# Performance work log

Hardware: AMD Instinct MI355X
Metric: run time of the kernel (lower is better)

The kernel has to match this reference:

```python
import jax, jax.numpy as jnp
import numpy as np
import math

EPS = 1e-06
H = W = 28


def _cell_id(cell):
    Hc, Wc = H // cell, W // cell
    yy = np.arange(H)[:, None]
    xx = np.arange(W)[None, :]
    cy = np.clip(yy // cell, 0, Hc - 1)
    cx = np.clip(xx // cell, 0, Wc - 1)
    return Hc, Wc, jnp.asarray((cy * Wc + cx).astype(np.int32))


def _sobel(x):
    # x: [B,1,28,28], zero-padded 3x3 Sobel, scaled by 1/4
    p = jnp.pad(x, ((0, 0), (0, 0), (1, 1), (1, 1)))
    gx = (p[..., :-2, :-2] + 2.0 * p[..., 1:-1, :-2] + p[..., 2:, :-2]
          - p[..., :-2, 2:] - 2.0 * p[..., 1:-1, 2:] - p[..., 2:, 2:]) * 0.25
    gy = (p[..., :-2, :-2] + 2.0 * p[..., :-2, 1:-1] + p[..., :-2, 2:]
          - p[..., 2:, :-2] - 2.0 * p[..., 2:, 1:-1] - p[..., 2:, 2:]) * 0.25
    return gx, gy


def _hog_generic(gx, gy, bins, cell, eps):
    B = gx.shape[0]
    mag = jnp.sqrt(gx * gx + gy * gy + eps)
    ang = jnp.arctan2(gy, gx) * (180.0 / math.pi)
    ang = (ang + 180.0) % 180.0
    Hc, Wc, cell_id = _cell_id(cell)
    bin_w = 180.0 / bins
    b0 = jnp.clip(jnp.floor(ang / bin_w), 0, bins - 1).astype(jnp.int32)
    frac = (ang - b0.astype(ang.dtype) * bin_w) / bin_w
    b1 = (b0 + 1) % bins
    base = (jnp.arange(B, dtype=jnp.int32) * (Hc * Wc)).reshape(B, 1, 1, 1)
    dest = base + cell_id[None, None, :, :]  # [B,1,H,W]
    m = mag.reshape(-1)
    f = frac.reshape(-1)
    d = dest.reshape(-1)
    idx0 = d * bins + b0.reshape(-1)
    idx1 = d * bins + b1.reshape(-1)
    nseg = B * Hc * Wc * bins
    # single fused scatter-add for both soft-assigned bins
    hist_1d = jax.ops.segment_sum(
        jnp.concatenate([m * (1.0 - f), m * f]),
        jnp.concatenate([idx0, idx1]),
        num_segments=nseg,
    )
    hist = hist_1d.reshape(B, Hc, Wc, bins)
    blk = jnp.stack(
        [hist[:, :-1, :-1, :], hist[:, :-1, 1:, :],
         hist[:, 1:, :-1, :], hist[:, 1:, 1:, :]],
        axis=-2,
    ).reshape(B, Hc - 1, Wc - 1, 4 * bins)
    norm = jnp.sqrt(jnp.sum(blk * blk, axis=-1, keepdims=True) + 1e-06)
    blk = jnp.minimum(blk / norm, 0.2)  # L2-hys clip
    norm2 = jnp.sqrt(jnp.sum(blk * blk, axis=-1, keepdims=True) + 1e-06)
    blk = blk / norm2
    return blk.reshape(B, -1)


def setup_inputs() -> dict:
    key = jax.random.key(0)
    k1, k2 = jax.random.split(key)
    B = 16384
    x = jax.random.uniform(k1, (B, 1, 28, 28), dtype=jnp.float32)
    feat_dim = 784 + 1152 + 2304 + 4056
    feat_mean = jnp.zeros((feat_dim,), dtype=jnp.float32)
    feat_std = jnp.ones((feat_dim,), dtype=jnp.float32)
    return {"x": x, "feat_mean": feat_mean, "feat_std": feat_std}


def reference(x, feat_mean, feat_std):
    x = x.astype(jnp.float32)
    gx, gy = _sobel(x)
    h4 = _hog_generic(gx, gy, bins=8, cell=4, eps=EPS)   # [B,1152]
    h3 = _hog_generic(gx, gy, bins=9, cell=3, eps=EPS)   # [B,2304]
    h2 = _hog_generic(gx, gy, bins=6, cell=2, eps=EPS)   # [B,4056]
    flat = x.reshape(x.shape[0], -1)                      # [B,784]
    feat = jnp.concatenate([flat, h4, h3, h2], axis=1)    # [B,8296]
    return (feat - feat_mean) / feat_std
```

## Files before the change

kernel.cpp:

```cpp
#include <hip/hip_runtime.h>
#include <hip/hip_fp16.h>
#include <math.h>


constexpr int NPIX = 784;
constexpr int FEAT = 8296;
constexpr int PB4 = 10, PB3 = 10, PB2 = 8;
constexpr int O4P = 0;
constexpr int O3P = 490;
constexpr int O2P = 1300;
constexpr int HIST_TOT = 2868;
constexpr int NTASK = 269;
constexpr int NHOG = FEAT - NPIX;
constexpr int NCELL = 49 + 81 + 196;

__device__ __forceinline__ int feat_map(int i) {
    int task, h;
    if (i < 1936) {
        int k = i - 784;
        int t = k >> 5, r = k & 31;
        int q = r >> 3, j = r & 7;
        int by = t / 6, bx = t - by * 6;
        h = O4P + ((by + (q >> 1)) * 7 + bx + (q & 1)) * PB4 + j;
        task = t;
    } else if (i < 4240) {
        int k = i - 1936;
        int t = k / 36, r = k - t * 36;
        int q = r / 9,  j = r - q * 9;
        int by = t >> 3, bx = t & 7;
        h = O3P + ((by + (q >> 1)) * 9 + bx + (q & 1)) * PB3 + j;
        task = 36 + t;
    } else {
        int k = i - 4240;
        int t = k / 24, r = k - t * 24;
        int q = r / 6,  j = r - q * 6;
        int by = t / 13, bx = t - by * 13;
        h = O2P + ((by + (q >> 1)) * 14 + bx + (q & 1)) * PB2 + j;
        task = 100 + t;
    }
    return (task << 12) | h;
}

__global__ __launch_bounds__(256)
void setup_kernel(const float* __restrict__ fmean,
                  const float* __restrict__ fstd,
                  float2* __restrict__ msr, int* __restrict__ map) {
    int i = blockIdx.x * 256 + threadIdx.x;
    if (i < FEAT) {
        msr[i] = make_float2(fmean[i], 1.0f / fstd[i]);
        if (i >= NPIX) map[i - NPIX] = feat_map(i);
    }
}

__device__ __forceinline__ float orient_deg(float gy, float gx) {
    float ax = fabsf(gx), ay = fabsf(gy);
    float mn = fminf(ax, ay), mx = fmaxf(ax, ay);
    float r = __fdividef(mn, mx + 1e-37f);
    float a = r * r;
    float th = ((((0.0208351f * a - 0.0851330f) * a + 0.1801410f) * a
                 - 0.3302995f) * a + 0.9998660f) * r;
    th *= 57.29577951308232f;
    if (ay > ax) th = 90.0f - th;
    bool neg = ((__float_as_uint(gx) ^ __float_as_uint(gy)) >> 31) != 0;
    float o = neg ? 180.0f - th : th;
    return (o >= 180.0f) ? 0.0f : o;
}

__device__ __forceinline__ float ldimg(const float* img, int y, int x) {
    return (y >= 0 && y < 28 && x >= 0 && x < 28) ? img[y * 28 + x] : 0.0f;
}

template <int BINS>
__device__ __forceinline__ float2 norm_task(const float* hist, int c00,
                                            int Wc, int pb) {
    int qb[4] = {c00, c00 + pb, c00 + Wc * pb, c00 + (Wc + 1) * pb};
    float s = 1e-6f;
    #pragma unroll
    for (int q = 0; q < 4; ++q) {
        #pragma unroll
        for (int j = 0; j < BINS / 2; ++j) {
            float2 v = *reinterpret_cast<const float2*>(&hist[qb[q] + 2 * j]);
            s += v.x * v.x + v.y * v.y;
        }
        if (BINS & 1) {
            float v = hist[qb[q] + BINS - 1];
            s += v * v;
        }
    }
    float ninv = 1.0f / sqrtf(s);
    float s2 = 1e-6f;
    #pragma unroll
    for (int q = 0; q < 4; ++q) {
        #pragma unroll
        for (int j = 0; j < BINS / 2; ++j) {
            float2 v = *reinterpret_cast<const float2*>(&hist[qb[q] + 2 * j]);
            float c0 = fminf(v.x * ninv, 0.2f);
            float c1 = fminf(v.y * ninv, 0.2f);
            s2 += c0 * c0 + c1 * c1;
        }
        if (BINS & 1) {
            float c = fminf(hist[qb[q] + BINS - 1] * ninv, 0.2f);
            s2 += c * c;
        }
    }
    return make_float2(ninv, 1.0f / sqrtf(s2));
}

template <bool USE_TABLE>
__global__ __launch_bounds__(256)
void hog_kernel(const float* __restrict__ x,
                const float* __restrict__ fmean,
                const float* __restrict__ fstd,
                const float2* __restrict__ msr,
                const int* __restrict__ map,
                float* __restrict__ out) {
    __shared__ __align__(16) float img[NPIX];
    __shared__ __align__(16) __half2 ma[NPIX];
    __shared__ __align__(16) float hist[HIST_TOT];
    __shared__ float2 nrm[NTASK];

    const int b = blockIdx.x;
    const int tid = threadIdx.x;
    const float* xb = x + (size_t)b * NPIX;

    for (int i = tid; i < NPIX / 4; i += 256)
        reinterpret_cast<float4*>(img)[i] =
            reinterpret_cast<const float4*>(xb)[i];
    for (int i = tid; i < HIST_TOT / 4; i += 256)
        reinterpret_cast<float4*>(hist)[i] = make_float4(0.f, 0.f, 0.f, 0.f);
    __syncthreads();

    for (int p = tid; p < NPIX; p += 256) {
        int y = p / 28, xx = p - (p / 28) * 28;
        float a00 = ldimg(img, y - 1, xx - 1);
        float a01 = ldimg(img, y - 1, xx);
        float a02 = ldimg(img, y - 1, xx + 1);
        float a10 = ldimg(img, y,     xx - 1);
        float a12 = ldimg(img, y,     xx + 1);
        float a20 = ldimg(img, y + 1, xx - 1);
        float a21 = ldimg(img, y + 1, xx);
        float a22 = ldimg(img, y + 1, xx + 1);
        float gxv = (a00 + 2.0f * a10 + a20 - a02 - 2.0f * a12 - a22) * 0.25f;
        float gyv = (a00 + 2.0f * a01 + a02 - a20 - 2.0f * a21 - a22) * 0.25f;
        float mag = sqrtf(gxv * gxv + gyv * gyv + 1e-6f);
        ma[p] = __floats2half2_rn(mag, orient_deg(gyv, gxv));
    }
    __syncthreads();

    for (int t = tid; t < NCELL; t += 256) {
        int base, y0, x0, ny, nx, bins;
        float invbw;
        if (t < 49) {
            int cy = t / 7, cx = t - cy * 7;
            y0 = cy * 4; x0 = cx * 4; ny = 4; nx = 4;
            bins = 8; invbw = 8.0f / 180.0f;
            base = O4P + t * PB4;
        } else if (t < 130) {
            int k = t - 49;
            int cy = k / 9, cx = k - cy * 9;
            y0 = cy * 3; x0 = cx * 3;
            ny = (cy == 8) ? 4 : 3; nx = (cx == 8) ? 4 : 3;
            bins = 9; invbw = 9.0f / 180.0f;
            base = O3P + k * PB3;
        } else {
            int k = t - 130;
            int cy = k / 14, cx = k - cy * 14;
            y0 = cy * 2; x0 = cx * 2; ny = 2; nx = 2;
            bins = 6; invbw = 6.0f / 180.0f;
            base = O2P + k * PB2;
        }
        for (int iy = 0; iy < ny; ++iy) {
            int row = (y0 + iy) * 28 + x0;
            for (int ix = 0; ix < nx; ++ix) {
                float2 m = __half22float2(ma[row + ix]);
                float tb = m.y * invbw;
                int b0 = (int)tb;
                if (b0 > bins - 1) b0 = bins - 1;
                float frac = tb - (float)b0;
                float w1 = m.x * frac;
                float w0 = m.x - w1;
                int a = base + b0;
                float h0 = hist[a];
                float h1 = hist[a + 1];
                hist[a]     = h0 + w0;
                hist[a + 1] = h1 + w1;
            }
        }
        hist[base] += hist[base + bins];
    }
    __syncthreads();

    for (int t = tid; t < NTASK; t += 256) {
        float2 r;
        if (t < 36) {
            int by = t / 6, bx = t - (t / 6) * 6;
            r = norm_task<8>(hist, O4P + (by * 7 + bx) * PB4, 7, PB4);
        } else if (t < 100) {
            int k = t - 36;
            r = norm_task<9>(hist, O3P + ((k >> 3) * 9 + (k & 7)) * PB3, 9, PB3);
        } else {
            int k = t - 100;
            int by = k / 13, bx = k - by * 13;
            r = norm_task<6>(hist, O2P + (by * 14 + bx) * PB2, 14, PB2);
        }
        nrm[t] = r;
    }
    __syncthreads();

    float4* outp = reinterpret_cast<float4*>(out + (size_t)b * FEAT);

    for (int i4 = tid; i4 < NPIX / 4; i4 += 256) {
        float4 v = reinterpret_cast<const float4*>(img)[i4];
        float4 r;
        if (USE_TABLE) {
            const float4* msr4 = reinterpret_cast<const float4*>(msr);
            float4 p0 = msr4[i4 * 2], p1 = msr4[i4 * 2 + 1];
            r.x = (v.x - p0.x) * p0.y;  r.y = (v.y - p0.z) * p0.w;
            r.z = (v.z - p1.x) * p1.y;  r.w = (v.w - p1.z) * p1.w;
        } else {
            int i = i4 * 4;
            r.x = (v.x - fmean[i])     / fstd[i];
            r.y = (v.y - fmean[i + 1]) / fstd[i + 1];
            r.z = (v.z - fmean[i + 2]) / fstd[i + 2];
            r.w = (v.w - fmean[i + 3]) / fstd[i + 3];
        }
        outp[i4] = r;
    }

    for (int t4 = tid; t4 < NHOG / 4; t4 += 256) {
        int i4 = NPIX / 4 + t4;
        int mp[4];
        if (USE_TABLE) {
            int4 m4 = reinterpret_cast<const int4*>(map)[t4];
            mp[0] = m4.x; mp[1] = m4.y; mp[2] = m4.z; mp[3] = m4.w;
        } else {
            #pragma unroll
            for (int e = 0; e < 4; ++e) mp[e] = feat_map(i4 * 4 + e);
        }
        float2 n = nrm[mp[0] >> 12];
        float vv[4];
        #pragma unroll
        for (int e = 0; e < 4; ++e)
            vv[e] = fminf(hist[mp[e] & 4095] * n.x, 0.2f) * n.y;
        float4 r;
        if (USE_TABLE) {
            const float4* msr4 = reinterpret_cast<const float4*>(msr);
            float4 p0 = msr4[i4 * 2], p1 = msr4[i4 * 2 + 1];
            r.x = (vv[0] - p0.x) * p0.y;  r.y = (vv[1] - p0.z) * p0.w;
            r.z = (vv[2] - p1.x) * p1.y;  r.w = (vv[3] - p1.z) * p1.w;
        } else {
            int i = i4 * 4;
            r.x = (vv[0] - fmean[i])     / fstd[i];
            r.y = (vv[1] - fmean[i + 1]) / fstd[i + 1];
            r.z = (vv[2] - fmean[i + 2]) / fstd[i + 2];
            r.w = (vv[3] - fmean[i + 3]) / fstd[i + 3];
        }
        outp[i4] = r;
    }
}

extern "C" void kernel_launch(void* const* d_in, const int* in_sizes, int n_in,
                              void* d_out, int out_size, void* d_ws, size_t ws_size,
                              hipStream_t stream) {
    const float* x     = (const float*)d_in[0];
    const float* fmean = (const float*)d_in[1];
    const float* fstd  = (const float*)d_in[2];
    float* out = (float*)d_out;
    int B = in_sizes[0] / NPIX;

    const size_t msr_bytes = (size_t)FEAT * sizeof(float2);
    const size_t map_bytes = (size_t)NHOG * sizeof(int);
    if (ws_size >= msr_bytes + map_bytes) {
        float2* msr = (float2*)d_ws;
        int* map = (int*)((char*)d_ws + msr_bytes);
        hipLaunchKernelGGL(setup_kernel, dim3((FEAT + 255) / 256), dim3(256),
                           0, stream, fmean, fstd, msr, map);
        hipLaunchKernelGGL(hog_kernel<true>, dim3(B), dim3(256), 0, stream,
                           x, fmean, fstd, msr, map, out);
    } else {
        hipLaunchKernelGGL(hog_kernel<false>, dim3(B), dim3(256), 0, stream,
                           x, fmean, fstd, nullptr, nullptr, out);
    }
}
```

Measured before the change: 185.4 us.

## Pad image in LDS, vectorize Sobel per 4 pixels, fuse pixel output, split HOG emit

The image is now stored in a zero-padded 30x32 shared buffer, so the Sobel stage needs no bounds checks. Each thread computes four adjacent pixels from vectorized row loads and writes packed half2 results. The raw-pixel normalized output is written during the initial load, and the per-block norms are stored as half2 to cut LDS use. The HOG emit loop is split into per-scale segments so the 8-bin and 6-bin scales read histogram pairs as float2. The fallback path without a workspace table is removed, and the half-precision norms can lower accuracy.

```diff
diff --git a/kernel.cpp b/kernel.cpp
--- a/kernel.cpp
+++ b/kernel.cpp
@@ -13,6 +13,7 @@
 constexpr int NTASK = 269;
 constexpr int NHOG = FEAT - NPIX;
 constexpr int NCELL = 49 + 81 + 196;
+constexpr int IMS = 32;
 
 __device__ __forceinline__ int feat_map(int i) {
     int task, h;
@@ -66,8 +67,8 @@
     return (o >= 180.0f) ? 0.0f : o;
 }
 
-__device__ __forceinline__ float ldimg(const float* img, int y, int x) {
-    return (y >= 0 && y < 28 && x >= 0 && x < 28) ? img[y * 28 + x] : 0.0f;
+__device__ __forceinline__ unsigned h2u(__half2 h) {
+    union { __half2 h; unsigned u; } v; v.h = h; return v.u;
 }
 
 template <int BINS>
@@ -107,6 +108,30 @@
 }
 
 template <bool USE_TABLE>
+__device__ __forceinline__ void emit4(float4* outp, const float4* msr4,
+                                      const float* fmean, const float* fstd,
+                                      int i4, float v0, float v1, float v2,
+                                      float v3, float2 n) {
+    v0 = fminf(v0 * n.x, 0.2f) * n.y;
+    v1 = fminf(v1 * n.x, 0.2f) * n.y;
+    v2 = fminf(v2 * n.x, 0.2f) * n.y;
+    v3 = fminf(v3 * n.x, 0.2f) * n.y;
+    float4 r;
+    if (USE_TABLE) {
+        float4 p0 = msr4[i4 * 2], p1 = msr4[i4 * 2 + 1];
+        r.x = (v0 - p0.x) * p0.y;  r.y = (v1 - p0.z) * p0.w;
+        r.z = (v2 - p1.x) * p1.y;  r.w = (v3 - p1.z) * p1.w;
+    } else {
+        int i = i4 * 4;
+        r.x = (v0 - fmean[i])     / fstd[i];
+        r.y = (v1 - fmean[i + 1]) / fstd[i + 1];
+        r.z = (v2 - fmean[i + 2]) / fstd[i + 2];
+        r.w = (v3 - fmean[i + 3]) / fstd[i + 3];
+    }
+    outp[i4] = r;
+}
+
+template <bool USE_TABLE>
 __global__ __launch_bounds__(256)
 void hog_kernel(const float* __restrict__ x,
                 const float* __restrict__ fmean,
@@ -114,36 +139,76 @@
                 const float2* __restrict__ msr,
                 const int* __restrict__ map,
                 float* __restrict__ out) {
-    __shared__ __align__(16) float img[NPIX];
+    __shared__ __align__(16) float img_p[30 * IMS];
     __shared__ __align__(16) __half2 ma[NPIX];
     __shared__ __align__(16) float hist[HIST_TOT];
-    __shared__ float2 nrm[NTASK];
+    __shared__ __half2 nrm[NTASK];
 
     const int b = blockIdx.x;
     const int tid = threadIdx.x;
     const float* xb = x + (size_t)b * NPIX;
-
-    for (int i = tid; i < NPIX / 4; i += 256)
-        reinterpret_cast<float4*>(img)[i] =
-            reinterpret_cast<const float4*>(xb)[i];
+    float4* outp = reinterpret_cast<float4*>(out + (size_t)b * FEAT);
+    const float4* msr4 = reinterpret_cast<const float4*>(msr);
+
+    for (int i = tid; i < 116; i += 256) {
+        int r, c;
+        if (i < 30)      { r = 0;      c = i;      }
+        else if (i < 60) { r = 29;     c = i - 30; }
+        else if (i < 88) { r = i - 59; c = 0;      }
+        else             { r = i - 87; c = 29;     }
+        img_p[r * IMS + c] = 0.0f;
+    }
     for (int i = tid; i < HIST_TOT / 4; i += 256)
         reinterpret_cast<float4*>(hist)[i] = make_float4(0.f, 0.f, 0.f, 0.f);
+    if (tid < 196) {
+        float4 v = reinterpret_cast<const float4*>(xb)[tid];
+        int y = tid / 7, c4 = (tid - y * 7) * 4;
+        float* dst = &img_p[(y + 1) * IMS + 1 + c4];
+        dst[0] = v.x; dst[1] = v.y; dst[2] = v.z; dst[3] = v.w;
+        float4 r;
+        if (USE_TABLE) {
+            float4 p0 = msr4[tid * 2], p1 = msr4[tid * 2 + 1];
+            r.x = (v.x - p0.x) * p0.y;  r.y = (v.y - p0.z) * p0.w;
+            r.z = (v.z - p1.x) * p1.y;  r.w = (v.w - p1.z) * p1.w;
+        } else {
+            int i = tid * 4;
+            r.x = (v.x - fmean[i])     / fstd[i];
+            r.y = (v.y - fmean[i + 1]) / fstd[i + 1];
+            r.z = (v.z - fmean[i + 2]) / fstd[i + 2];
+            r.w = (v.w - fmean[i + 3]) / fstd[i + 3];
+        }
+        outp[tid] = r;
+    }
     __syncthreads();
 
-    for (int p = tid; p < NPIX; p += 256) {
-        int y = p / 28, xx = p - (p / 28) * 28;
-        float a00 = ldimg(img, y - 1, xx - 1);
-        float a01 = ldimg(img, y - 1, xx);
-        float a02 = ldimg(img, y - 1, xx + 1);
-        float a10 = ldimg(img, y,     xx - 1);
-        float a12 = ldimg(img, y,     xx + 1);
-        float a20 = ldimg(img, y + 1, xx - 1);
-        float a21 = ldimg(img, y + 1, xx);
-        float a22 = ldimg(img, y + 1, xx + 1);
-        float gxv = (a00 + 2.0f * a10 + a20 - a02 - 2.0f * a12 - a22) * 0.25f;
-        float gyv = (a00 + 2.0f * a01 + a02 - a20 - 2.0f * a21 - a22) * 0.25f;
-        float mag = sqrtf(gxv * gxv + gyv * gyv + 1e-6f);
-        ma[p] = __floats2half2_rn(mag, orient_deg(gyv, gxv));
+    if (tid < 196) {
+        int y = tid / 7, x0 = (tid - (tid / 7) * 7) * 4;
+        const float* r0 = &img_p[y * IMS + x0];
+        const float* r1 = r0 + IMS;
+        const float* r2 = r1 + IMS;
+        float4 q0 = *reinterpret_cast<const float4*>(r0);
+        float2 s0 = *reinterpret_cast<const float2*>(r0 + 4);
+        float4 q1 = *reinterpret_cast<const float4*>(r1);
+        float2 s1 = *reinterpret_cast<const float2*>(r1 + 4);
+        float4 q2 = *reinterpret_cast<const float4*>(r2);
+        float2 s2 = *reinterpret_cast<const float2*>(r2 + 4);
+        float A0[6] = {q0.x, q0.y, q0.z, q0.w, s0.x, s0.y};
+        float A1[6] = {q1.x, q1.y, q1.z, q1.w, s1.x, s1.y};
+        float A2[6] = {q2.x, q2.y, q2.z, q2.w, s2.x, s2.y};
+        unsigned mo[4];
+        #pragma unroll
+        for (int i = 0; i < 4; ++i) {
+            float a00 = A0[i], a01 = A0[i + 1], a02 = A0[i + 2];
+            float a10 = A1[i],                  a12 = A1[i + 2];
+            float a20 = A2[i], a21 = A2[i + 1], a22 = A2[i + 2];
+            float gxv = (a00 + 2.0f * a10 + a20 - a02 - 2.0f * a12 - a22) * 0.25f;
+            float gyv = (a00 + 2.0f * a01 + a02 - a20 - 2.0f * a21 - a22) * 0.25f;
+            float mag = sqrtf(gxv * gxv + gyv * gyv + 1e-6f);
+            mo[i] = h2u(__floats2half2_rn(mag, orient_deg(gyv, gxv)));
+        }
+        int p0 = y * 28 + x0;
+        reinterpret_cast<uint4*>(ma)[p0 >> 2] =
+            make_uint4(mo[0], mo[1], mo[2], mo[3]);
     }
     __syncthreads();
 
@@ -203,61 +268,40 @@
             int by = k / 13, bx = k - by * 13;
             r = norm_task<6>(hist, O2P + (by * 14 + bx) * PB2, 14, PB2);
         }
-        nrm[t] = r;
+        nrm[t] = __floats2half2_rn(r.x, r.y);
     }
     __syncthreads();
 
-    float4* outp = reinterpret_cast<float4*>(out + (size_t)b * FEAT);
-
-    for (int i4 = tid; i4 < NPIX / 4; i4 += 256) {
-        float4 v = reinterpret_cast<const float4*>(img)[i4];
-        float4 r;
-        if (USE_TABLE) {
-            const float4* msr4 = reinterpret_cast<const float4*>(msr);
-            float4 p0 = msr4[i4 * 2], p1 = msr4[i4 * 2 + 1];
-            r.x = (v.x - p0.x) * p0.y;  r.y = (v.y - p0.z) * p0.w;
-            r.z = (v.z - p1.x) * p1.y;  r.w = (v.w - p1.z) * p1.w;
-        } else {
-            int i = i4 * 4;
-            r.x = (v.x - fmean[i])     / fstd[i];
-            r.y = (v.y - fmean[i + 1]) / fstd[i + 1];
-            r.z = (v.z - fmean[i + 2]) / fstd[i + 2];
-            r.w = (v.w - fmean[i + 3]) / fstd[i + 3];
-        }
-        outp[i4] = r;
-    }
-
-    for (int t4 = tid; t4 < NHOG / 4; t4 += 256) {
-        int i4 = NPIX / 4 + t4;
-        int mp[4];
-        if (USE_TABLE) {
-            int4 m4 = reinterpret_cast<const int4*>(map)[t4];
-            mp[0] = m4.x; mp[1] = m4.y; mp[2] = m4.z; mp[3] = m4.w;
-        } else {
-            #pragma unroll
-            for (int e = 0; e < 4; ++e) mp[e] = feat_map(i4 * 4 + e);
-        }
-        float2 n = nrm[mp[0] >> 12];
-        float vv[4];
-        #pragma unroll
-        for (int e = 0; e < 4; ++e)
-            vv[e] = fminf(hist[mp[e] & 4095] * n.x, 0.2f) * n.y;
-        float4 r;
-        if (USE_TABLE) {
-            const float4* msr4 = reinterpret_cast<const float4*>(msr);
-            float4 p0 = msr4[i4 * 2], p1 = msr4[i4 * 2 + 1];
-            r.x = (vv[0] - p0.x) * p0.y;  r.y = (vv[1] - p0.z) * p0.w;
-            r.z = (vv[2] - p1.x) * p1.y;  r.w = (vv[3] - p1.z) * p1.w;
-        } else {
-            int i = i4 * 4;
-            r.x = (vv[0] - fmean[i])     / fstd[i];
-            r.y = (vv[1] - fmean[i + 1]) / fstd[i + 1];
-            r.z = (vv[2] - fmean[i + 2]) / fstd[i + 2];
-            r.w = (vv[3] - fmean[i + 3]) / fstd[i + 3];
-        }
-        outp[i4] = r;
-    }
-}
+    const int4* map4 = reinterpret_cast<const int4*>(map);
+
+    for (int t4 = tid; t4 < 288; t4 += 256) {
+        int i4 = 196 + t4;
+        int4 m4 = map4[t4];
+        float2 n = __half22float2(nrm[m4.x >> 12]);
+        float2 v01 = *reinterpret_cast<const float2*>(&hist[m4.x & 4095]);
+        float2 v23 = *reinterpret_cast<const float2*>(&hist[m4.z & 4095]);
+        emit4<USE_TABLE>(outp, msr4, fmean, fstd, i4,
+                         v01.x, v01.y, v23.x, v23.y, n);
+    }
+    for (int t4 = 288 + tid; t4 < 864; t4 += 256) {
+        int i4 = 196 + t4;
+        int4 m4 = map4[t4];
+        float2 n = __half22float2(nrm[m4.x >> 12]);
+        float v0 = hist[m4.x & 4095], v1 = hist[m4.y & 4095];
+        float v2 = hist[m4.z & 4095], v3 = hist[m4.w & 4095];
+        emit4<USE_TABLE>(outp, msr4, fmean, fstd, i4, v0, v1, v2, v3, n);
+    }
+    for (int t4 = 864 + tid; t4 < NHOG / 4; t4 += 256) {
+        int i4 = 196 + t4;
+        int4 m4 = map4[t4];
+        float2 n = __half22float2(nrm[m4.x >> 12]);
+        float2 v01 = *reinterpret_cast<const float2*>(&hist[m4.x & 4095]);
+        float2 v23 = *reinterpret_cast<const float2*>(&hist[m4.z & 4095]);
+        emit4<USE_TABLE>(outp, msr4, fmean, fstd, i4,
+                         v01.x, v01.y, v23.x, v23.y, n);
+    }
+}
+
 
 extern "C" void kernel_launch(void* const* d_in, const int* in_sizes, int n_in,
                               void* d_out, int out_size, void* d_ws, size_t ws_size,
@@ -270,15 +314,11 @@
 
     const size_t msr_bytes = (size_t)FEAT * sizeof(float2);
     const size_t map_bytes = (size_t)NHOG * sizeof(int);
-    if (ws_size >= msr_bytes + map_bytes) {
-        float2* msr = (float2*)d_ws;
-        int* map = (int*)((char*)d_ws + msr_bytes);
-        hipLaunchKernelGGL(setup_kernel, dim3((FEAT + 255) / 256), dim3(256),
-                           0, stream, fmean, fstd, msr, map);
-        hipLaunchKernelGGL(hog_kernel<true>, dim3(B), dim3(256), 0, stream,
-                           x, fmean, fstd, msr, map, out);
-    } else {
-        hipLaunchKernelGGL(hog_kernel<false>, dim3(B), dim3(256), 0, stream,
-                           x, fmean, fstd, nullptr, nullptr, out);
-    }
-}
+    float2* msr = (float2*)d_ws;
+    int* map = (int*)((char*)d_ws + msr_bytes);
+    (void)msr_bytes; (void)map_bytes;
+    hipLaunchKernelGGL(setup_kernel, dim3((FEAT + 255) / 256), dim3(256),
+                       0, stream, fmean, fstd, msr, map);
+    hipLaunchKernelGGL(hog_kernel<true>, dim3(B), dim3(256), 0, stream,
+                       x, fmean, fstd, msr, map, out);
+}
```

After: 217.2 us. 17.1% more time.

## Process eight images per block with double-buffered histograms overlapping output writes

Applied to the files above, without the earlier changes.

Each block now handles eight images in sequence. Histograms and norm buffers are double-buffered so the HOG output stores for one image are issued alongside loading and histogramming the next. Norm factors are stored as half2 to save LDS, which may cost a little precision. The block count drops eightfold, which reduces parallelism and adds LDS per block.

```diff
diff --git a/kernel.cpp b/kernel.cpp
--- a/kernel.cpp
+++ b/kernel.cpp
@@ -70,66 +70,19 @@
     return (y >= 0 && y < 28 && x >= 0 && x < 28) ? img[y * 28 + x] : 0.0f;
 }
 
-template <int BINS>
-__device__ __forceinline__ float2 norm_task(const float* hist, int c00,
-                                            int Wc, int pb) {
-    int qb[4] = {c00, c00 + pb, c00 + Wc * pb, c00 + (Wc + 1) * pb};
-    float s = 1e-6f;
-    #pragma unroll
-    for (int q = 0; q < 4; ++q) {
-        #pragma unroll
-        for (int j = 0; j < BINS / 2; ++j) {
-            float2 v = *reinterpret_cast<const float2*>(&hist[qb[q] + 2 * j]);
-            s += v.x * v.x + v.y * v.y;
-        }
-        if (BINS & 1) {
-            float v = hist[qb[q] + BINS - 1];
-            s += v * v;
-        }
-    }
-    float ninv = 1.0f / sqrtf(s);
-    float s2 = 1e-6f;
-    #pragma unroll
-    for (int q = 0; q < 4; ++q) {
-        #pragma unroll
-        for (int j = 0; j < BINS / 2; ++j) {
-            float2 v = *reinterpret_cast<const float2*>(&hist[qb[q] + 2 * j]);
-            float c0 = fminf(v.x * ninv, 0.2f);
-            float c1 = fminf(v.y * ninv, 0.2f);
-            s2 += c0 * c0 + c1 * c1;
-        }
-        if (BINS & 1) {
-            float c = fminf(hist[qb[q] + BINS - 1] * ninv, 0.2f);
-            s2 += c * c;
-        }
-    }
-    return make_float2(ninv, 1.0f / sqrtf(s2));
-}
-
-template <bool USE_TABLE>
-__global__ __launch_bounds__(256)
-void hog_kernel(const float* __restrict__ x,
-                const float* __restrict__ fmean,
-                const float* __restrict__ fstd,
-                const float2* __restrict__ msr,
-                const int* __restrict__ map,
-                float* __restrict__ out) {
-    __shared__ __align__(16) float img[NPIX];
-    __shared__ __align__(16) __half2 ma[NPIX];
-    __shared__ __align__(16) float hist[HIST_TOT];
-    __shared__ float2 nrm[NTASK];
-
-    const int b = blockIdx.x;
-    const int tid = threadIdx.x;
-    const float* xb = x + (size_t)b * NPIX;
-
+
+__device__ __forceinline__ void phaseA(const float* __restrict__ xb,
+                                       float* __restrict__ img,
+                                       float* __restrict__ histb, int tid) {
     for (int i = tid; i < NPIX / 4; i += 256)
         reinterpret_cast<float4*>(img)[i] =
             reinterpret_cast<const float4*>(xb)[i];
     for (int i = tid; i < HIST_TOT / 4; i += 256)
-        reinterpret_cast<float4*>(hist)[i] = make_float4(0.f, 0.f, 0.f, 0.f);
-    __syncthreads();
-
+        reinterpret_cast<float4*>(histb)[i] = make_float4(0.f, 0.f, 0.f, 0.f);
+}
+
+__device__ __forceinline__ void phaseB(const float* __restrict__ img,
+                                       __half2* __restrict__ ma, int tid) {
     for (int p = tid; p < NPIX; p += 256) {
         int y = p / 28, xx = p - (p / 28) * 28;
         float a00 = ldimg(img, y - 1, xx - 1);
@@ -145,8 +98,10 @@
         float mag = sqrtf(gxv * gxv + gyv * gyv + 1e-6f);
         ma[p] = __floats2half2_rn(mag, orient_deg(gyv, gxv));
     }
-    __syncthreads();
-
+}
+
+__device__ __forceinline__ void phaseC(const __half2* __restrict__ ma,
+                                       float* __restrict__ histb, int tid) {
     for (int t = tid; t < NCELL; t += 256) {
         int base, y0, x0, ny, nx, bins;
         float invbw;
@@ -180,40 +135,80 @@
                 float w1 = m.x * frac;
                 float w0 = m.x - w1;
                 int a = base + b0;
-                float h0 = hist[a];
-                float h1 = hist[a + 1];
-                hist[a]     = h0 + w0;
-                hist[a + 1] = h1 + w1;
+                float h0 = histb[a];
+                float h1 = histb[a + 1];
+                histb[a]     = h0 + w0;
+                histb[a + 1] = h1 + w1;
             }
         }
-        hist[base] += hist[base + bins];
-    }
-    __syncthreads();
-
+        histb[base] += histb[base + bins];
+    }
+}
+
+template <int BINS>
+__device__ __forceinline__ float2 norm_task(const float* hist, int c00,
+                                            int Wc, int pb) {
+    int qb[4] = {c00, c00 + pb, c00 + Wc * pb, c00 + (Wc + 1) * pb};
+    float s = 1e-6f;
+    #pragma unroll
+    for (int q = 0; q < 4; ++q) {
+        #pragma unroll
+        for (int j = 0; j < BINS / 2; ++j) {
+            float2 v = *reinterpret_cast<const float2*>(&hist[qb[q] + 2 * j]);
+            s += v.x * v.x + v.y * v.y;
+        }
+        if (BINS & 1) {
+            float v = hist[qb[q] + BINS - 1];
+            s += v * v;
+        }
+    }
+    float ninv = 1.0f / sqrtf(s);
+    float s2 = 1e-6f;
+    #pragma unroll
+    for (int q = 0; q < 4; ++q) {
+        #pragma unroll
+        for (int j = 0; j < BINS / 2; ++j) {
+            float2 v = *reinterpret_cast<const float2*>(&hist[qb[q] + 2 * j]);
+            float c0 = fminf(v.x * ninv, 0.2f);
+            float c1 = fminf(v.y * ninv, 0.2f);
+            s2 += c0 * c0 + c1 * c1;
+        }
+        if (BINS & 1) {
+            float c = fminf(hist[qb[q] + BINS - 1] * ninv, 0.2f);
+            s2 += c * c;
+        }
+    }
+    return make_float2(ninv, 1.0f / sqrtf(s2));
+}
+
+template <bool USE_TABLE>
+__device__ __forceinline__ void phaseD_flat(const float* __restrict__ histb,
+                                            __half2* __restrict__ nrmb,
+                                            const float* __restrict__ img,
+                                            float4* __restrict__ outp,
+                                            const float4* __restrict__ msr4,
+                                            const float* __restrict__ fmean,
+                                            const float* __restrict__ fstd,
+                                            int tid) {
     for (int t = tid; t < NTASK; t += 256) {
         float2 r;
         if (t < 36) {
             int by = t / 6, bx = t - (t / 6) * 6;
-            r = norm_task<8>(hist, O4P + (by * 7 + bx) * PB4, 7, PB4);
+            r = norm_task<8>(histb, O4P + (by * 7 + bx) * PB4, 7, PB4);
         } else if (t < 100) {
             int k = t - 36;
-            r = norm_task<9>(hist, O3P + ((k >> 3) * 9 + (k & 7)) * PB3, 9, PB3);
+            r = norm_task<9>(histb, O3P + ((k >> 3) * 9 + (k & 7)) * PB3, 9, PB3);
         } else {
             int k = t - 100;
             int by = k / 13, bx = k - by * 13;
-            r = norm_task<6>(hist, O2P + (by * 14 + bx) * PB2, 14, PB2);
-        }
-        nrm[t] = r;
-    }
-    __syncthreads();
-
-    float4* outp = reinterpret_cast<float4*>(out + (size_t)b * FEAT);
-
+            r = norm_task<6>(histb, O2P + (by * 14 + bx) * PB2, 14, PB2);
+        }
+        nrmb[t] = __floats2half2_rn(r.x, r.y);
+    }
     for (int i4 = tid; i4 < NPIX / 4; i4 += 256) {
         float4 v = reinterpret_cast<const float4*>(img)[i4];
         float4 r;
         if (USE_TABLE) {
-            const float4* msr4 = reinterpret_cast<const float4*>(msr);
             float4 p0 = msr4[i4 * 2], p1 = msr4[i4 * 2 + 1];
             r.x = (v.x - p0.x) * p0.y;  r.y = (v.y - p0.z) * p0.w;
             r.z = (v.z - p1.x) * p1.y;  r.w = (v.w - p1.z) * p1.w;
@@ -226,7 +221,17 @@
         }
         outp[i4] = r;
     }
-
+}
+
+template <bool USE_TABLE>
+__device__ __forceinline__ void ehog(const float* __restrict__ histb,
+                                     const __half2* __restrict__ nrmb,
+                                     float4* __restrict__ outp,
+                                     const int* __restrict__ map,
+                                     const float4* __restrict__ msr4,
+                                     const float* __restrict__ fmean,
+                                     const float* __restrict__ fstd,
+                                     int tid) {
     for (int t4 = tid; t4 < NHOG / 4; t4 += 256) {
         int i4 = NPIX / 4 + t4;
         int mp[4];
@@ -237,14 +242,13 @@
             #pragma unroll
             for (int e = 0; e < 4; ++e) mp[e] = feat_map(i4 * 4 + e);
         }
-        float2 n = nrm[mp[0] >> 12];
+        float2 n = __half22float2(nrmb[mp[0] >> 12]);
         float vv[4];
         #pragma unroll
         for (int e = 0; e < 4; ++e)
-            vv[e] = fminf(hist[mp[e] & 4095] * n.x, 0.2f) * n.y;
+            vv[e] = fminf(histb[mp[e] & 4095] * n.x, 0.2f) * n.y;
         float4 r;
         if (USE_TABLE) {
-            const float4* msr4 = reinterpret_cast<const float4*>(msr);
             float4 p0 = msr4[i4 * 2], p1 = msr4[i4 * 2 + 1];
             r.x = (vv[0] - p0.x) * p0.y;  r.y = (vv[1] - p0.z) * p0.w;
             r.z = (vv[2] - p1.x) * p1.y;  r.w = (vv[3] - p1.z) * p1.w;
@@ -256,6 +260,57 @@
             r.w = (vv[3] - fmean[i + 3]) / fstd[i + 3];
         }
         outp[i4] = r;
+    }
+}
+
+template <bool USE_TABLE, int NIMG>
+__global__ __launch_bounds__(256)
+void hog_kernel(const float* __restrict__ x,
+                const float* __restrict__ fmean,
+                const float* __restrict__ fstd,
+                const float2* __restrict__ msr,
+                const int* __restrict__ map,
+                float* __restrict__ out) {
+    __shared__ __align__(16) float img[NPIX];
+    __shared__ __align__(16) __half2 ma[NPIX];
+    __shared__ __align__(16) float hist[2][HIST_TOT];
+    __shared__ __align__(16) __half2 nrm[2][NTASK];
+
+    const int tid = threadIdx.x;
+    const size_t i0 = (size_t)blockIdx.x * NIMG;
+    const float4* msr4 = reinterpret_cast<const float4*>(msr);
+
+    int p = 0;
+    phaseA(x + i0 * NPIX, img, hist[0], tid);
+    __syncthreads();
+    phaseB(img, ma, tid);
+    __syncthreads();
+    phaseC(ma, hist[0], tid);
+    __syncthreads();
+    phaseD_flat<USE_TABLE>(hist[0], nrm[0], img,
+                           reinterpret_cast<float4*>(out + i0 * FEAT),
+                           msr4, fmean, fstd, tid);
+    __syncthreads();
+
+    for (int k = 0; k < NIMG; ++k) {
+        float4* outk = reinterpret_cast<float4*>(out + (i0 + k) * FEAT);
+        if (k + 1 < NIMG) {
+            phaseA(x + (i0 + k + 1) * NPIX, img, hist[1 - p], tid);
+            ehog<USE_TABLE>(hist[p], nrm[p], outk, map, msr4, fmean, fstd, tid);
+            __syncthreads();
+            phaseB(img, ma, tid);
+            __syncthreads();
+            phaseC(ma, hist[1 - p], tid);
+            __syncthreads();
+            phaseD_flat<USE_TABLE>(hist[1 - p], nrm[1 - p], img,
+                                   reinterpret_cast<float4*>(
+                                       out + (i0 + k + 1) * FEAT),
+                                   msr4, fmean, fstd, tid);
+            __syncthreads();
+            p ^= 1;
+        } else {
+            ehog<USE_TABLE>(hist[p], nrm[p], outk, map, msr4, fmean, fstd, tid);
+        }
     }
 }
 
@@ -270,15 +325,26 @@
 
     const size_t msr_bytes = (size_t)FEAT * sizeof(float2);
     const size_t map_bytes = (size_t)NHOG * sizeof(int);
-    if (ws_size >= msr_bytes + map_bytes) {
-        float2* msr = (float2*)d_ws;
-        int* map = (int*)((char*)d_ws + msr_bytes);
+    bool tables = ws_size >= msr_bytes + map_bytes;
+    float2* msr = (float2*)d_ws;
+    int* map = (int*)((char*)d_ws + msr_bytes);
+    if (tables)
         hipLaunchKernelGGL(setup_kernel, dim3((FEAT + 255) / 256), dim3(256),
                            0, stream, fmean, fstd, msr, map);
-        hipLaunchKernelGGL(hog_kernel<true>, dim3(B), dim3(256), 0, stream,
-                           x, fmean, fstd, msr, map, out);
+
+    if ((B % 8) == 0) {
+        if (tables)
+            hipLaunchKernelGGL((hog_kernel<true, 8>), dim3(B / 8), dim3(256),
+                               0, stream, x, fmean, fstd, msr, map, out);
+        else
+            hipLaunchKernelGGL((hog_kernel<false, 8>), dim3(B / 8), dim3(256),
+                               0, stream, x, fmean, fstd, nullptr, nullptr, out);
     } else {
-        hipLaunchKernelGGL(hog_kernel<false>, dim3(B), dim3(256), 0, stream,
-                           x, fmean, fstd, nullptr, nullptr, out);
-    }
-}
+        if (tables)
+            hipLaunchKernelGGL((hog_kernel<true, 1>), dim3(B), dim3(256),
+                               0, stream, x, fmean, fstd, msr, map, out);
+        else
+            hipLaunchKernelGGL((hog_kernel<false, 1>), dim3(B), dim3(256),
+                               0, stream, x, fmean, fstd, nullptr, nullptr, out);
+    }
+}
```

Result: slower. 254.8 us (+37.4%).
